# Performance work log

Hardware: AMD Instinct MI355X
Metric: run time of the kernel (lower is better)

## Reference

```python
import jax, jax.numpy as jnp
import numpy as np
import math

N_POLY = 300
N_DEG = 3
OUT_DIM = 2 * (N_DEG + 1)  # 8 sampled points per query
HEADS = 8


def _grid_sample(x, grid):
    # x: [B,C,H,W], grid: [B,Q,N,2] in [-1,1]; bilinear, zeros padding, align_corners=False
    B, C, H, W = x.shape
    ix = (grid[..., 0] + 1.0) * (W * 0.5) - 0.5
    iy = (grid[..., 1] + 1.0) * (H * 0.5) - 0.5
    ix0 = jnp.floor(ix)
    iy0 = jnp.floor(iy)
    wx1 = ix - ix0
    wy1 = iy - iy0
    x0 = ix0.astype(jnp.int32)
    y0 = iy0.astype(jnp.int32)
    xf = x.reshape(B, C, H * W)

    def gather(yc, xc):
        valid = (xc >= 0) & (xc < W) & (yc >= 0) & (yc < H)
        idx = jnp.clip(yc, 0, H - 1) * W + jnp.clip(xc, 0, W - 1)  # [B,Q,N]
        vals = jax.vmap(lambda m, i: m[:, i])(xf, idx)  # [B,C,Q,N]
        return vals * valid[:, None].astype(x.dtype)

    out = (gather(y0, x0) * ((1 - wy1) * (1 - wx1))[:, None]
           + gather(y0, x0 + 1) * ((1 - wy1) * wx1)[:, None]
           + gather(y0 + 1, x0) * (wy1 * (1 - wx1))[:, None]
           + gather(y0 + 1, x0 + 1) * (wy1 * wx1)[:, None])
    return out  # [B,C,Q,N]


def setup_inputs() -> dict:
    key = jax.random.key(0)
    B, C, H, W = 16, 256, 64, 96
    ks = list(jax.random.split(key, 20))

    def w(k, shape):
        return jax.random.normal(k, shape, jnp.float32) * (1.0 / np.sqrt(shape[0]))

    d = {}
    d['x'] = jax.random.normal(ks[0], (B, C, H, W), jnp.float32)
    d['qs_w1'] = w(ks[1], (C, 2 * C)); d['qs_b1'] = jnp.zeros((2 * C,), jnp.float32)
    d['qs_w2'] = w(ks[2], (2 * C, 1)); d['qs_b2'] = jnp.zeros((1,), jnp.float32)
    d['rp_w1'] = w(ks[3], (C, 2 * C)); d['rp_b1'] = jnp.zeros((2 * C,), jnp.float32)
    d['rp_w2'] = w(ks[4], (2 * C, OUT_DIM * 2)); d['rp_b2'] = jnp.zeros((OUT_DIM * 2,), jnp.float32)
    d['mha_in_w'] = w(ks[5], (C, 3 * C)); d['mha_in_b'] = jnp.zeros((3 * C,), jnp.float32)
    d['mha_out_w'] = w(ks[6], (C, C)); d['mha_out_b'] = jnp.zeros((C,), jnp.float32)
    d['dq_w'] = w(ks[7], (C, C)); d['dq_b'] = jnp.zeros((C,), jnp.float32)
    d['dk_w'] = w(ks[8], (C, C)); d['dk_b'] = jnp.zeros((C,), jnp.float32)
    d['dv_w'] = w(ks[9], (C, C)); d['dv_b'] = jnp.zeros((C,), jnp.float32)
    d['ln1_g'] = jnp.ones((C,), jnp.float32); d['ln1_b'] = jnp.zeros((C,), jnp.float32)
    d['cl_w1'] = w(ks[10], (C, 2 * C)); d['cl_b1'] = jnp.zeros((2 * C,), jnp.float32)
    d['cl_w2'] = w(ks[11], (2 * C, 1)); d['cl_b2'] = jnp.zeros((1,), jnp.float32)
    d['po_w1'] = w(ks[12], (C, 2 * C)); d['po_b1'] = jnp.zeros((2 * C,), jnp.float32)
    d['po_w2'] = w(ks[13], (2 * C, OUT_DIM)); d['po_b2'] = jnp.zeros((OUT_DIM,), jnp.float32)
    return d


def reference(x, qs_w1, qs_b1, qs_w2, qs_b2, rp_w1, rp_b1, rp_w2, rp_b2,
              mha_in_w, mha_in_b, mha_out_w, mha_out_b,
              dq_w, dq_b, dk_w, dk_b, dv_w, dv_b,
              ln1_g, ln1_b, cl_w1, cl_b1, cl_w2, cl_b2,
              po_w1, po_b1, po_w2, po_b2):
    B, C, H, W = x.shape
    dh = C // HEADS
    scale = 1.0 / math.sqrt(dh)

    memory = x.reshape(B, C, H * W).transpose(0, 2, 1)  # [B,HW,C]
    logits = jax.nn.elu(memory @ qs_w1 + qs_b1) @ qs_w2 + qs_b2  # [B,HW,1]
    _, idxs = jax.lax.top_k(logits[..., 0], N_POLY)  # [B,Q]
    querys = jnp.take_along_axis(memory, idxs[..., None], axis=1)  # [B,Q,C]
    rp = jnp.tanh((memory @ rp_w1 + rp_b1) @ rp_w2 + rp_b2)  # [B,HW,2*OUT_DIM]
    ref = jnp.take_along_axis(rp, idxs[..., None], axis=1).reshape(B, N_POLY, OUT_DIM, 2)

    # self-attention (nn.MultiheadAttention, batch_first, 8 heads)
    qkv = querys @ mha_in_w + mha_in_b
    q, k, v = jnp.split(qkv, 3, axis=-1)
    sh = lambda t: t.reshape(B, N_POLY, HEADS, dh).transpose(0, 2, 1, 3)
    q, k, v = sh(q), sh(k), sh(v)
    att = jax.nn.softmax(jnp.einsum('bhqd,bhkd->bhqk', q, k) * scale, axis=-1)
    o = jnp.einsum('bhqk,bhkd->bhqd', att, v).transpose(0, 2, 1, 3).reshape(B, N_POLY, C)
    o = o @ mha_out_w + mha_out_b
    tgt = querys + o  # dropout is identity in eval
    mu = tgt.mean(-1, keepdims=True)
    var = tgt.var(-1, keepdims=True)
    tgt = (tgt - mu) / jnp.sqrt(var + 1e-5) * ln1_g + ln1_b

    # deformable attention
    dq = (tgt @ dq_w + dq_b).reshape(B, N_POLY, 1, HEADS, dh).transpose(0, 1, 3, 2, 4)  # [B,Q,H,1,dh]
    samp = _grid_sample(x, ref)  # [B,C,Q,N]
    sp = samp.transpose(0, 3, 2, 1)  # [B,N,Q,C] (matches torch transpose(1,-1))
    # faithful to torch .view(B,Q,N,H,dh) on the [B,N,Q,C] contiguous tensor: plain reshape
    dk = (sp @ dk_w + dk_b).reshape(B, N_POLY, OUT_DIM, HEADS, dh).transpose(0, 1, 3, 2, 4)  # [B,Q,H,N,dh]
    dv = (sp @ dv_w + dv_b).reshape(B, N_POLY, OUT_DIM, HEADS, dh).transpose(0, 1, 3, 2, 4)
    a = jax.nn.softmax(jnp.einsum('bqhod,bqhnd->bqhon', dq, dk) * scale, axis=-1)
    out2 = jnp.einsum('bqhon,bqhnd->bqhod', a, dv).reshape(B, N_POLY, C)
    tgt = tgt + out2

    poly = jax.nn.silu(tgt @ po_w1 + po_b1) @ po_w2 + po_b2
    cls = jax.nn.sigmoid(jax.nn.elu(tgt @ cl_w1 + cl_b1) @ cl_w2 + cl_b2)[..., 0]
    return poly.reshape(B, N_POLY, 2, N_DEG + 1), cls
```

## Files before the change

kernel.cpp:

```cpp
#include <hip/hip_runtime.h>
#include <hip/hip_bf16.h>
#include <math.h>

typedef __hip_bfloat16 bf16;

#define B_   16
#define C_   256
#define H_   64
#define W_   96
#define HW_  6144
#define Q_   300
#define NH_  8
#define DH_  32
#define HID_ 512
#define QB_  4
#define SCALE_ 0.17677669529663687f

__device__ __forceinline__ float b2f(bf16 v){ return __bfloat162float(v); }
__device__ __forceinline__ bf16 f2b(float v){ return __float2bfloat16(v); }
__device__ __forceinline__ int clampi(int v, int lo, int hi){
  return v < lo ? lo : (v > hi ? hi : v);
}

__global__ __launch_bounds__(256) void xt_k(const float* __restrict__ x,
                                            float* __restrict__ xt){
  int b  = blockIdx.z;
  int c0 = blockIdx.y*64;
  int p0 = blockIdx.x*64;
  __shared__ float t[64][65];
  int tid = threadIdx.x;
  int tr = tid >> 6;
  int tc = tid & 63;
  #pragma unroll
  for (int i=0;i<16;i++){
    int cc = tr + i*4;
    t[cc][tc] = x[((size_t)b*C_ + c0+cc)*HW_ + p0 + tc];
  }
  __syncthreads();
  #pragma unroll
  for (int i=0;i<16;i++){
    int pp = tr + i*4;
    xt[((size_t)b*HW_ + p0+pp)*C_ + c0 + tc] = t[tc][pp];
  }
}

__global__ __launch_bounds__(256) void score_k(const float* __restrict__ x,
    const float* __restrict__ w1, const float* __restrict__ b1,
    const float* __restrict__ w2, const float* __restrict__ b2,
    float* __restrict__ logits){
  int b = blockIdx.y, hw0 = blockIdx.x*64;
  int tid = threadIdx.x;
  int tc = tid & 31;
  int tr = tid >> 5;
  __shared__ float xs[32][64];
  __shared__ float wsl[32][256];
  __shared__ float red[64][33];
  float part[8];
  #pragma unroll
  for (int i=0;i<8;i++) part[i]=0.f;
  for (int pass=0; pass<2; ++pass){
    float acc[8][8];
    #pragma unroll
    for (int i=0;i<8;i++)
      #pragma unroll
      for (int j=0;j<8;j++) acc[i][j]=0.f;
    for (int kt=0; kt<8; ++kt){
      #pragma unroll
      for (int i=0;i<2;i++){
        int e = tid + i*256;
        int rr4 = e & 15, kk = e >> 4;
        *reinterpret_cast<float4*>(&xs[kk][rr4*4]) =
          *reinterpret_cast<const float4*>(&x[(size_t)(b*C_ + kt*32+kk)*HW_ + hw0 + rr4*4]);
      }
      #pragma unroll
      for (int i=0;i<8;i++){
        int e = tid + i*256;
        int jj4 = e & 63, kk = e >> 6;
        *reinterpret_cast<float4*>(&wsl[kk][jj4*4]) =
          *reinterpret_cast<const float4*>(&w1[(size_t)(kt*32+kk)*HID_ + pass*256 + jj4*4]);
      }
      __syncthreads();
      #pragma unroll
      for (int k=0;k<32;k++){
        float4 a0 = *reinterpret_cast<float4*>(&xs[k][tr*8]);
        float4 a1 = *reinterpret_cast<float4*>(&xs[k][tr*8+4]);
        float4 w0 = *reinterpret_cast<float4*>(&wsl[k][tc*8]);
        float4 w4 = *reinterpret_cast<float4*>(&wsl[k][tc*8+4]);
        float aa[8] = {a0.x,a0.y,a0.z,a0.w,a1.x,a1.y,a1.z,a1.w};
        float ww[8] = {w0.x,w0.y,w0.z,w0.w,w4.x,w4.y,w4.z,w4.w};
        #pragma unroll
        for (int i=0;i<8;i++)
          #pragma unroll
          for (int j=0;j<8;j++)
            acc[i][j] += aa[i]*ww[j];
      }
      __syncthreads();
    }
    #pragma unroll
    for (int j=0;j<8;j++){
      int jg = pass*256 + tc*8 + j;
      float bb = b1[jg], w2v = w2[jg];
      #pragma unroll
      for (int i=0;i<8;i++){
        float h = acc[i][j] + bb;
        h = h > 0.f ? h : expm1f(h);
        part[i] += h * w2v;
      }
    }
  }
  #pragma unroll
  for (int i=0;i<8;i++) red[tr*8+i][tc] = part[i];
  __syncthreads();
  if (tid < 64){
    float s = 0.f;
    for (int t=0;t<32;t++) s += red[tid][t];
    logits[(size_t)b*HW_ + hw0 + tid] = s + b2[0];
  }
}

__global__ __launch_bounds__(1024) void topk_k(const float* __restrict__ logits,
                                               int* __restrict__ idxs){
  int b = blockIdx.x, tid = threadIdx.x;
  __shared__ unsigned long long keys[8192];
  for (int i = tid; i < 8192; i += 1024){
    unsigned long long key = 0ull;
    if (i < HW_){
      float v = logits[(size_t)b*HW_ + i];
      unsigned u = __float_as_uint(v);
      unsigned m = (u & 0x80000000u) ? ~u : (u ^ 0x80000000u);
      if (!(v == v)) m = 0u;
      key = ((unsigned long long)m << 32) | (unsigned)(HW_ - 1 - i);
    }
    keys[i] = key;
  }
  __syncthreads();
  for (int k = 2; k <= 8192; k <<= 1){
    for (int j = k >> 1; j >= 1; j >>= 1){
      for (int i = tid; i < 8192; i += 1024){
        int l = i ^ j;
        if (l > i){
          unsigned long long a = keys[i], c = keys[l];
          bool sw = ((i & k) == 0) ? (a < c) : (a > c);
          if (sw){ keys[i] = c; keys[l] = a; }
        }
      }
      __syncthreads();
    }
  }
  if (tid < Q_){
    int idx = HW_ - 1 - (int)(keys[tid] & 0xFFFFFFFFull);
    idxs[b*Q_ + tid] = idx;
  }
}

template<int XT>
__global__ __launch_bounds__(256) void qproj_k(const float* __restrict__ x,
    const float* __restrict__ xt,
    const int* __restrict__ idxs,
    const float* __restrict__ rw1, const float* __restrict__ rb1,
    const float* __restrict__ rw2, const float* __restrict__ rb2,
    const float* __restrict__ mw,  const float* __restrict__ mb,
    float* __restrict__ refs,
    bf16* __restrict__ qarr, bf16* __restrict__ karr, bf16* __restrict__ varr){
  int blk = blockIdx.x;
  int b = blk/(Q_/QB_), q0 = (blk%(Q_/QB_))*QB_;
  int tid = threadIdx.x;
  __shared__ float rowl[QB_][C_];
  __shared__ float hl[QB_][HID_];
  __shared__ float red[16][17];
  int idxv[QB_];
  #pragma unroll
  for (int j=0;j<QB_;j++) idxv[j] = clampi(idxs[b*Q_+q0+j], 0, HW_-1);
  #pragma unroll
  for (int j=0;j<QB_;j++){
    if (XT) rowl[j][tid] = xt[((size_t)b*HW_ + idxv[j])*C_ + tid];
    else    rowl[j][tid] = x[((size_t)b*C_ + tid)*HW_ + idxv[j]];
  }
  __syncthreads();
  float h0[QB_], h1[QB_];
  #pragma unroll
  for (int j=0;j<QB_;j++){ h0[j]=rb1[tid]; h1[j]=rb1[tid+256]; }
  for (int c=0;c<C_;c++){
    float wv0 = rw1[(size_t)c*HID_ + tid];
    float wv1 = rw1[(size_t)c*HID_ + tid + 256];
    #pragma unroll
    for (int j=0;j<QB_;j++){
      float rv = rowl[j][c];
      h0[j] += rv*wv0; h1[j] += rv*wv1;
    }
  }
  #pragma unroll
  for (int j=0;j<QB_;j++){ hl[j][tid]=h0[j]; hl[j][tid+256]=h1[j]; }
  float aq[QB_], ak[QB_], av[QB_];
  #pragma unroll
  for (int j=0;j<QB_;j++){ aq[j]=mb[tid]; ak[j]=mb[tid+256]; av[j]=mb[tid+512]; }
  for (int c=0;c<C_;c++){
    const float* wr = mw + (size_t)c*768;
    float w0 = wr[tid], w1v = wr[tid+256], w2v = wr[tid+512];
    #pragma unroll
    for (int j=0;j<QB_;j++){
      float rv = rowl[j][c];
      aq[j] += rv*w0; ak[j] += rv*w1v; av[j] += rv*w2v;
    }
  }
  int h = tid>>5, d = tid&31;
  #pragma unroll
  for (int j=0;j<QB_;j++){
    size_t o = (((size_t)b*NH_+h)*Q_+(q0+j))*DH_ + d;
    qarr[o]=f2b(aq[j]); karr[o]=f2b(ak[j]); varr[o]=f2b(av[j]);
  }
  __syncthreads();
  int o = tid & 15, seg = tid >> 4;
  for (int j=0;j<QB_;j++){
    float p = 0.f;
    for (int jj=seg*32; jj<seg*32+32; jj++) p += hl[j][jj]*rw2[jj*16+o];
    red[seg][o] = p;
    __syncthreads();
    if (tid < 16){
      float s = 0.f;
      for (int sg=0; sg<16; sg++) s += red[sg][tid];
      refs[((size_t)b*Q_+(q0+j))*16 + tid] = tanhf(s + rb2[tid]);
    }
    __syncthreads();
  }
}

__global__ __launch_bounds__(256) void attn_k(const bf16* __restrict__ qarr,
    const bf16* __restrict__ karr, const bf16* __restrict__ varr,
    bf16* __restrict__ att_o){
  int blk = blockIdx.x; int bh = blk >> 1, half = blk & 1;
  int tid = threadIdx.x, rg = tid >> 5, lane = tid & 31;
  __shared__ bf16 kk[Q_][34];
  __shared__ bf16 vv[Q_][34];
  __shared__ float ps[8][304];
  __shared__ float qsl[8][32];
  const bf16* kb = karr + (size_t)bh*Q_*DH_;
  const bf16* vb = varr + (size_t)bh*Q_*DH_;
  const bf16* qb = qarr + (size_t)bh*Q_*DH_;
  for (int e=tid; e<Q_*DH_; e+=256){
    int k = e >> 5, d = e & 31;
    kk[k][d] = kb[e];
    vv[k][d] = vb[e];
  }
  __syncthreads();
  int b = bh >> 3, h = bh & 7;
  int rbase = half*150;
  for (int p0=0; p0<150; p0+=8){
    int rr = p0 + rg;
    bool act = rr < 150;
    int r = rbase + (act ? rr : 0);
    float qd = act ? b2f(qb[r*DH_ + lane]) : 0.f;
    qsl[rg][lane] = qd;
    __syncthreads();
    float lmax = -1e30f;
    for (int k=lane; k<Q_; k+=32){
      float s = 0.f;
      #pragma unroll
      for (int d=0; d<DH_; d++) s += qsl[rg][d]*b2f(kk[k][d]);
      s *= SCALE_;
      ps[rg][k] = s;
      lmax = fmaxf(lmax, s);
    }
    #pragma unroll
    for (int off=16; off>=1; off>>=1) lmax = fmaxf(lmax, __shfl_xor(lmax, off, 32));
    float lsum = 0.f;
    for (int k=lane; k<Q_; k+=32){
      float e = expf(ps[rg][k] - lmax);
      ps[rg][k] = e;
      lsum += e;
    }
    #pragma unroll
    for (int off=16; off>=1; off>>=1) lsum += __shfl_xor(lsum, off, 32);
    __syncthreads();
    float out = 0.f;
    for (int k=0;k<Q_;k++) out += ps[rg][k]*b2f(vv[k][lane]);
    if (act) att_o[((size_t)b*Q_ + r)*C_ + h*DH_ + lane] = f2b(out / lsum);
    __syncthreads();
  }
}

template<int XT>
__global__ __launch_bounds__(256) void proj_ln_k(const bf16* __restrict__ att_o,
    const float* __restrict__ x, const float* __restrict__ xt,
    const int* __restrict__ idxs,
    const float* __restrict__ ow, const float* __restrict__ ob,
    const float* __restrict__ g,  const float* __restrict__ beta,
    const float* __restrict__ dqw, const float* __restrict__ dqb,
    float* __restrict__ tgt, float* __restrict__ dqv){
  int blk = blockIdx.x, tid = threadIdx.x;
  int b = blk/Q_, qq = blk%Q_;
  __shared__ float ol[C_];
  __shared__ float yl[C_];
  __shared__ float rs[4], rs2[4];
  size_t base = (size_t)blk*C_;
  ol[tid] = b2f(att_o[base+tid]);
  __syncthreads();
  float acc = ob[tid];
  for (int c=0;c<C_;c++) acc += ol[c]*ow[(size_t)c*C_+tid];
  int idx = clampi(idxs[b*Q_+qq], 0, HW_-1);
  float resid;
  if (XT) resid = xt[((size_t)b*HW_ + idx)*C_ + tid];
  else    resid = x[((size_t)b*C_ + tid)*HW_ + idx];
  float t = resid + acc;
  float s = t, s2 = t*t;
  #pragma unroll
  for (int off=32; off>=1; off>>=1){
    s  += __shfl_xor(s,  off, 64);
    s2 += __shfl_xor(s2, off, 64);
  }
  if ((tid&63)==0){ rs[tid>>6]=s; rs2[tid>>6]=s2; }
  __syncthreads();
  float ts=0.f, ts2=0.f;
  #pragma unroll
  for (int w=0;w<4;w++){ ts+=rs[w]; ts2+=rs2[w]; }
  float mu = ts*(1.f/256.f);
  float var = ts2*(1.f/256.f) - mu*mu;
  if (!(var > 0.f)) var = 0.f;
  float y = (t-mu)*rsqrtf(var+1e-5f)*g[tid] + beta[tid];
  tgt[base+tid] = y;
  yl[tid] = y;
  __syncthreads();
  float a2 = dqb[tid];
  for (int c=0;c<C_;c++) a2 += yl[c]*dqw[(size_t)c*C_+tid];
  dqv[base+tid] = a2;
}

template<int XT>
__global__ __launch_bounds__(256) void deform_k(const float* __restrict__ x,
    const float* __restrict__ xt,
    const float* __restrict__ refs, const float* __restrict__ dqv,
    const float* __restrict__ tgt,
    const float* __restrict__ dkw, const float* __restrict__ dkb,
    const float* __restrict__ dvw, const float* __restrict__ dvb,
    const float* __restrict__ pw1, const float* __restrict__ pb1,
    const float* __restrict__ pw2, const float* __restrict__ pb2,
    const float* __restrict__ cw1, const float* __restrict__ cb1,
    const float* __restrict__ cw2, const float* __restrict__ cb2,
    float* __restrict__ out_poly, float* __restrict__ out_cls){
  int blk = blockIdx.x; int b = blk/Q_, q2 = blk%Q_;
  int tid = threadIdx.x;
  __shared__ float rows_l[8][C_];
  __shared__ float k8[8][C_];
  __shared__ float v8[8][C_];
  __shared__ float dql[C_];
  __shared__ float tl[C_];
  __shared__ float hp[HID_];
  __shared__ float hc[HID_];
  __shared__ float redp[16][8];
  __shared__ float redc[16];
  dql[tid] = dqv[((size_t)b*Q_+q2)*C_ + tid];
  const float* xc  = x  + ((size_t)b*C_ + tid)*HW_;
  const float* xbt = xt + (size_t)b*HW_*C_;
  #pragma unroll
  for (int rr=0; rr<8; ++rr){
    int r = q2*8 + rr;
    int n = r/Q_, q = r - n*Q_;
    float gx = refs[(((size_t)b*Q_+q)*8+n)*2 + 0];
    float gy = refs[(((size_t)b*Q_+q)*8+n)*2 + 1];
    if (!(gx > -2.f && gx < 2.f)) gx = 0.f;
    if (!(gy > -2.f && gy < 2.f)) gy = 0.f;
    float ix = (gx + 1.f)*48.f - 0.5f;
    float iy = (gy + 1.f)*32.f - 0.5f;
    float fx = floorf(ix), fy = floorf(iy);
    int x0 = (int)fx, y0 = (int)fy;
    float wx1 = ix - fx, wy1 = iy - fy;
    float wx0 = 1.f - wx1, wy0 = 1.f - wy1;
    float v = 0.f;
    if (XT){
      if (y0   >= 0 && y0   < H_ && x0   >= 0 && x0   < W_) v += wy0*wx0*xbt[(size_t)(y0*W_+x0)*C_ + tid];
      if (y0   >= 0 && y0   < H_ && x0+1 >= 0 && x0+1 < W_) v += wy0*wx1*xbt[(size_t)(y0*W_+x0+1)*C_ + tid];
      if (y0+1 >= 0 && y0+1 < H_ && x0   >= 0 && x0   < W_) v += wy1*wx0*xbt[(size_t)((y0+1)*W_+x0)*C_ + tid];
      if (y0+1 >= 0 && y0+1 < H_ && x0+1 >= 0 && x0+1 < W_) v += wy1*wx1*xbt[(size_t)((y0+1)*W_+x0+1)*C_ + tid];
    } else {
      if (y0   >= 0 && y0   < H_ && x0   >= 0 && x0   < W_) v += wy0*wx0*xc[y0*W_+x0];
      if (y0   >= 0 && y0   < H_ && x0+1 >= 0 && x0+1 < W_) v += wy0*wx1*xc[y0*W_+x0+1];
      if (y0+1 >= 0 && y0+1 < H_ && x0   >= 0 && x0   < W_) v += wy1*wx0*xc[(y0+1)*W_+x0];
      if (y0+1 >= 0 && y0+1 < H_ && x0+1 >= 0 && x0+1 < W_) v += wy1*wx1*xc[(y0+1)*W_+x0+1];
    }
    rows_l[rr][tid] = v;
  }
  __syncthreads();
  float ka[8], va[8];
  float kbb = dkb[tid], vbb = dvb[tid];
  #pragma unroll
  for (int rr=0; rr<8; ++rr){ ka[rr]=kbb; va[rr]=vbb; }
  for (int c=0;c<C_;c++){
    float wk = dkw[(size_t)c*C_+tid];
    float wvv = dvw[(size_t)c*C_+tid];
    #pragma unroll
    for (int rr=0; rr<8; ++rr){
      float rv = rows_l[rr][c];
      ka[rr] += rv*wk; va[rr] += rv*wvv;
    }
  }
  #pragma unroll
  for (int rr=0; rr<8; ++rr){ k8[rr][tid]=ka[rr]; v8[rr][tid]=va[rr]; }
  __syncthreads();
  int h = tid>>5, d = tid&31;
  float qd = dql[h*DH_+d];
  float s[8];
  #pragma unroll
  for (int n=0;n<8;n++){
    float t_ = qd * k8[n][h*DH_+d];
    #pragma unroll
    for (int off=16; off>=1; off>>=1) t_ += __shfl_xor(t_, off, 32);
    s[n] = t_ * SCALE_;
  }
  float m = s[0];
  #pragma unroll
  for (int n=1;n<8;n++) m = fmaxf(m, s[n]);
  float e[8], sum = 0.f;
  #pragma unroll
  for (int n=0;n<8;n++){ e[n] = expf(s[n]-m); sum += e[n]; }
  float inv = 1.f/sum;
  float out = 0.f;
  #pragma unroll
  for (int n=0;n<8;n++) out += e[n]*inv*v8[n][h*DH_+d];
  float tv = tgt[((size_t)b*Q_+q2)*C_ + tid] + out;
  tl[tid] = tv;
  __syncthreads();
  float a0 = pb1[tid], a1 = pb1[tid+256];
  float c0 = cb1[tid], c1 = cb1[tid+256];
  for (int c=0;c<C_;c++){
    float rv = tl[c];
    a0 += rv*pw1[(size_t)c*HID_ + tid];
    a1 += rv*pw1[(size_t)c*HID_ + tid + 256];
    c0 += rv*cw1[(size_t)c*HID_ + tid];
    c1 += rv*cw1[(size_t)c*HID_ + tid + 256];
  }
  hp[tid]     = a0 * (1.f/(1.f+expf(-a0)));
  hp[tid+256] = a1 * (1.f/(1.f+expf(-a1)));
  hc[tid]     = c0 > 0.f ? c0 : expm1f(c0);
  hc[tid+256] = c1 > 0.f ? c1 : expm1f(c1);
  __syncthreads();
  if (tid < 128){
    int o = tid & 7, seg = tid >> 3;
    float p = 0.f;
    for (int j=seg*32; j<seg*32+32; j++) p += hp[j]*pw2[j*8+o];
    redp[seg][o] = p;
  } else if (tid < 144){
    int seg = tid - 128;
    float p = 0.f;
    for (int j=seg*32; j<seg*32+32; j++) p += hc[j]*cw2[j];
    redc[seg] = p;
  }
  __syncthreads();
  if (tid < 8){
    float sm = 0.f;
    for (int sg=0; sg<16; sg++) sm += redp[sg][tid];
    out_poly[((size_t)b*Q_+q2)*8 + tid] = sm + pb2[tid];
  }
  if (tid == 8){
    float sc = 0.f;
    for (int sg=0; sg<16; sg++) sc += redc[sg];
    sc += cb2[0];
    out_cls[b*Q_+q2] = 1.f/(1.f+expf(-sc));
  }
}

extern "C" void kernel_launch(void* const* d_in, const int* in_sizes, int n_in,
                              void* d_out, int out_size, void* d_ws, size_t ws_size,
                              hipStream_t stream){
  (void)in_sizes; (void)out_size;
  if (n_in < 29) return;
  const float* x       = (const float*)d_in[0];
  const float* qs_w1   = (const float*)d_in[1];
  const float* qs_b1   = (const float*)d_in[2];
  const float* qs_w2   = (const float*)d_in[3];
  const float* qs_b2   = (const float*)d_in[4];
  const float* rp_w1   = (const float*)d_in[5];
  const float* rp_b1   = (const float*)d_in[6];
  const float* rp_w2   = (const float*)d_in[7];
  const float* rp_b2   = (const float*)d_in[8];
  const float* mha_in_w  = (const float*)d_in[9];
  const float* mha_in_b  = (const float*)d_in[10];
  const float* mha_out_w = (const float*)d_in[11];
  const float* mha_out_b = (const float*)d_in[12];
  const float* dq_w    = (const float*)d_in[13];
  const float* dq_b    = (const float*)d_in[14];
  const float* dk_w    = (const float*)d_in[15];
  const float* dk_b    = (const float*)d_in[16];
  const float* dv_w    = (const float*)d_in[17];
  const float* dv_b    = (const float*)d_in[18];
  const float* ln1_g   = (const float*)d_in[19];
  const float* ln1_b   = (const float*)d_in[20];
  const float* cl_w1   = (const float*)d_in[21];
  const float* cl_b1   = (const float*)d_in[22];
  const float* cl_w2   = (const float*)d_in[23];
  const float* cl_b2   = (const float*)d_in[24];
  const float* po_w1   = (const float*)d_in[25];
  const float* po_b1   = (const float*)d_in[26];
  const float* po_w2   = (const float*)d_in[27];
  const float* po_b2   = (const float*)d_in[28];

  constexpr size_t QKV1     = (size_t)B_*NH_*Q_*DH_;
  constexpr size_t SZ_R1    = 9830400;
  constexpr size_t OFF_IDXS = SZ_R1;
  constexpr size_t OFF_REFS = OFF_IDXS + 19200;
  constexpr size_t OFF_ATTO = OFF_REFS + 307200;
  constexpr size_t WS_NEED  = OFF_ATTO + 2457600;
  constexpr size_t OFF_XT   = WS_NEED;
  constexpr size_t SZ_XT    = (size_t)B_*HW_*C_*sizeof(float);
  constexpr size_t WS_NEED2 = OFF_XT + SZ_XT;
  if (ws_size < WS_NEED) return;
  const bool use_xt = (ws_size >= WS_NEED2);

  char* ws = (char*)d_ws;
  float* logits = (float*)(ws + 0);
  bf16*  qarr   = (bf16*) (ws + 0);
  bf16*  karr   = qarr + QKV1;
  bf16*  varr   = karr + QKV1;
  float* tgt    = (float*)(ws + 0);
  float* dqv    = (float*)(ws + 4915200);
  int*   idxs   = (int*)  (ws + OFF_IDXS);
  float* refs   = (float*)(ws + OFF_REFS);
  bf16*  att_o  = (bf16*) (ws + OFF_ATTO);
  float* xt     = (float*)(ws + OFF_XT);

  float* out_poly = (float*)d_out;
  float* out_cls  = out_poly + B_*Q_*8;

  if (use_xt)
    xt_k<<<dim3(HW_/64, C_/64, B_), 256, 0, stream>>>(x, xt);

  score_k<<<dim3(HW_/64, B_), 256, 0, stream>>>(x, qs_w1, qs_b1, qs_w2, qs_b2, logits);
  topk_k<<<B_, 1024, 0, stream>>>(logits, idxs);

  if (use_xt){
    qproj_k<1><<<B_*(Q_/QB_), 256, 0, stream>>>(x, xt, idxs, rp_w1, rp_b1, rp_w2, rp_b2,
                                                mha_in_w, mha_in_b, refs, qarr, karr, varr);
  } else {
    qproj_k<0><<<B_*(Q_/QB_), 256, 0, stream>>>(x, xt, idxs, rp_w1, rp_b1, rp_w2, rp_b2,
                                                mha_in_w, mha_in_b, refs, qarr, karr, varr);
  }
  attn_k<<<B_*NH_*2, 256, 0, stream>>>(qarr, karr, varr, att_o);
  if (use_xt){
    proj_ln_k<1><<<B_*Q_, 256, 0, stream>>>(att_o, x, xt, idxs, mha_out_w, mha_out_b,
                                            ln1_g, ln1_b, dq_w, dq_b, tgt, dqv);
    deform_k<1><<<B_*Q_, 256, 0, stream>>>(x, xt, refs, dqv, tgt,
                                           dk_w, dk_b, dv_w, dv_b,
                                           po_w1, po_b1, po_w2, po_b2,
                                           cl_w1, cl_b1, cl_w2, cl_b2,
                                           out_poly, out_cls);
  } else {
    proj_ln_k<0><<<B_*Q_, 256, 0, stream>>>(att_o, x, xt, idxs, mha_out_w, mha_out_b,
                                            ln1_g, ln1_b, dq_w, dq_b, tgt, dqv);
    deform_k<0><<<B_*Q_, 256, 0, stream>>>(x, xt, refs, dqv, tgt,
                                           dk_w, dk_b, dv_w, dv_b,
                                           po_w1, po_b1, po_w2, po_b2,
                                           cl_w1, cl_b1, cl_w2, cl_b2,
                                           out_poly, out_cls);
  }
}
```

Before: 1.276 ms.

## Batch four queries per deform block and remove LDS bank conflicts in score_k

deform_k now handles QB_=4 queries per block. Each dk/dv and MLP weight load is reused across 32 sampled rows or 4 queries instead of 8 rows or 1 query. This is meant to cut the repeated global weight traffic that dominates these matrix-vector products. The cost is higher register and LDS use (32-entry accumulators) and four times fewer blocks. Separately, score_k pads the xs tile and splits each thread's weight columns into two 4-wide halves to avoid LDS bank conflicts, and it reuses the weight tile buffer for the reduction to save shared memory.

```diff
diff --git a/kernel.cpp b/kernel.cpp
--- a/kernel.cpp
+++ b/kernel.cpp
@@ -52,9 +52,9 @@
   int tid = threadIdx.x;
   int tc = tid & 31;
   int tr = tid >> 5;
-  __shared__ float xs[32][64];
+  __shared__ float xs[32][68];
   __shared__ float wsl[32][256];
-  __shared__ float red[64][33];
+  float (*red)[33] = (float(*)[33])wsl;
   float part[8];
   #pragma unroll
   for (int i=0;i<8;i++) part[i]=0.f;
@@ -84,8 +84,8 @@
       for (int k=0;k<32;k++){
         float4 a0 = *reinterpret_cast<float4*>(&xs[k][tr*8]);
         float4 a1 = *reinterpret_cast<float4*>(&xs[k][tr*8+4]);
-        float4 w0 = *reinterpret_cast<float4*>(&wsl[k][tc*8]);
-        float4 w4 = *reinterpret_cast<float4*>(&wsl[k][tc*8+4]);
+        float4 w0 = *reinterpret_cast<float4*>(&wsl[k][tc*4]);
+        float4 w4 = *reinterpret_cast<float4*>(&wsl[k][128 + tc*4]);
         float aa[8] = {a0.x,a0.y,a0.z,a0.w,a1.x,a1.y,a1.z,a1.w};
         float ww[8] = {w0.x,w0.y,w0.z,w0.w,w4.x,w4.y,w4.z,w4.w};
         #pragma unroll
@@ -98,7 +98,8 @@
     }
     #pragma unroll
     for (int j=0;j<8;j++){
-      int jg = pass*256 + tc*8 + j;
+      int col = (j < 4) ? (tc*4 + j) : (128 + tc*4 + (j-4));
+      int jg = pass*256 + col;
       float bb = b1[jg], w2v = w2[jg];
       #pragma unroll
       for (int i=0;i<8;i++){
@@ -337,23 +338,19 @@
     const float* __restrict__ cw1, const float* __restrict__ cb1,
     const float* __restrict__ cw2, const float* __restrict__ cb2,
     float* __restrict__ out_poly, float* __restrict__ out_cls){
-  int blk = blockIdx.x; int b = blk/Q_, q2 = blk%Q_;
+  int blk = blockIdx.x; int b = blk/(Q_/QB_), qg = blk%(Q_/QB_);
+  int q0 = qg*QB_;
   int tid = threadIdx.x;
-  __shared__ float rows_l[8][C_];
-  __shared__ float k8[8][C_];
-  __shared__ float v8[8][C_];
-  __shared__ float dql[C_];
-  __shared__ float tl[C_];
-  __shared__ float hp[HID_];
-  __shared__ float hc[HID_];
+  __shared__ float rows_l[32][C_];
+  __shared__ float tl[QB_][C_];
+  __shared__ float hp[QB_][HID_];
+  __shared__ float hc[QB_][HID_];
   __shared__ float redp[16][8];
   __shared__ float redc[16];
-  dql[tid] = dqv[((size_t)b*Q_+q2)*C_ + tid];
   const float* xc  = x  + ((size_t)b*C_ + tid)*HW_;
   const float* xbt = xt + (size_t)b*HW_*C_;
-  #pragma unroll
-  for (int rr=0; rr<8; ++rr){
-    int r = q2*8 + rr;
+  for (int rloc=0; rloc<32; ++rloc){
+    int r = qg*32 + rloc;
     int n = r/Q_, q = r - n*Q_;
     float gx = refs[(((size_t)b*Q_+q)*8+n)*2 + 0];
     float gy = refs[(((size_t)b*Q_+q)*8+n)*2 + 1];
@@ -377,84 +374,101 @@
       if (y0+1 >= 0 && y0+1 < H_ && x0   >= 0 && x0   < W_) v += wy1*wx0*xc[(y0+1)*W_+x0];
       if (y0+1 >= 0 && y0+1 < H_ && x0+1 >= 0 && x0+1 < W_) v += wy1*wx1*xc[(y0+1)*W_+x0+1];
     }
-    rows_l[rr][tid] = v;
-  }
-  __syncthreads();
-  float ka[8], va[8];
+    rows_l[rloc][tid] = v;
+  }
+  __syncthreads();
+  float ka[32], va[32];
   float kbb = dkb[tid], vbb = dvb[tid];
   #pragma unroll
-  for (int rr=0; rr<8; ++rr){ ka[rr]=kbb; va[rr]=vbb; }
+  for (int rr=0; rr<32; ++rr){ ka[rr]=kbb; va[rr]=vbb; }
+  for (int c=0; c<C_; c+=4){
+    float wk0 = dkw[(size_t)(c+0)*C_+tid], wk1 = dkw[(size_t)(c+1)*C_+tid];
+    float wk2 = dkw[(size_t)(c+2)*C_+tid], wk3 = dkw[(size_t)(c+3)*C_+tid];
+    float wv0 = dvw[(size_t)(c+0)*C_+tid], wv1 = dvw[(size_t)(c+1)*C_+tid];
+    float wv2 = dvw[(size_t)(c+2)*C_+tid], wv3 = dvw[(size_t)(c+3)*C_+tid];
+    #pragma unroll
+    for (int rr=0; rr<32; ++rr){
+      float4 rv = *reinterpret_cast<float4*>(&rows_l[rr][c]);
+      ka[rr] += rv.x*wk0 + rv.y*wk1 + rv.z*wk2 + rv.w*wk3;
+      va[rr] += rv.x*wv0 + rv.y*wv1 + rv.z*wv2 + rv.w*wv3;
+    }
+  }
+  #pragma unroll
+  for (int jj=0; jj<QB_; ++jj){
+    int q2 = q0 + jj;
+    float qd = dqv[((size_t)b*Q_+q2)*C_ + tid];
+    float s[8];
+    #pragma unroll
+    for (int n=0;n<8;n++){
+      float t_ = qd * ka[jj*8+n];
+      #pragma unroll
+      for (int off=16; off>=1; off>>=1) t_ += __shfl_xor(t_, off, 32);
+      s[n] = t_ * SCALE_;
+    }
+    float m = s[0];
+    #pragma unroll
+    for (int n=1;n<8;n++) m = fmaxf(m, s[n]);
+    float e[8], sum = 0.f;
+    #pragma unroll
+    for (int n=0;n<8;n++){ e[n] = expf(s[n]-m); sum += e[n]; }
+    float inv = 1.f/sum;
+    float out = 0.f;
+    #pragma unroll
+    for (int n=0;n<8;n++) out += e[n]*inv*va[jj*8+n];
+    tl[jj][tid] = tgt[((size_t)b*Q_+q2)*C_ + tid] + out;
+  }
+  __syncthreads();
+  float a0[QB_], a1[QB_], c0[QB_], c1[QB_];
+  #pragma unroll
+  for (int jj=0;jj<QB_;jj++){
+    a0[jj]=pb1[tid]; a1[jj]=pb1[tid+256];
+    c0[jj]=cb1[tid]; c1[jj]=cb1[tid+256];
+  }
   for (int c=0;c<C_;c++){
-    float wk = dkw[(size_t)c*C_+tid];
-    float wvv = dvw[(size_t)c*C_+tid];
-    #pragma unroll
-    for (int rr=0; rr<8; ++rr){
-      float rv = rows_l[rr][c];
-      ka[rr] += rv*wk; va[rr] += rv*wvv;
-    }
-  }
-  #pragma unroll
-  for (int rr=0; rr<8; ++rr){ k8[rr][tid]=ka[rr]; v8[rr][tid]=va[rr]; }
-  __syncthreads();
-  int h = tid>>5, d = tid&31;
-  float qd = dql[h*DH_+d];
-  float s[8];
-  #pragma unroll
-  for (int n=0;n<8;n++){
-    float t_ = qd * k8[n][h*DH_+d];
-    #pragma unroll
-    for (int off=16; off>=1; off>>=1) t_ += __shfl_xor(t_, off, 32);
-    s[n] = t_ * SCALE_;
-  }
-  float m = s[0];
-  #pragma unroll
-  for (int n=1;n<8;n++) m = fmaxf(m, s[n]);
-  float e[8], sum = 0.f;
-  #pragma unroll
-  for (int n=0;n<8;n++){ e[n] = expf(s[n]-m); sum += e[n]; }
-  float inv = 1.f/sum;
-  float out = 0.f;
-  #pragma unroll
-  for (int n=0;n<8;n++) out += e[n]*inv*v8[n][h*DH_+d];
-  float tv = tgt[((size_t)b*Q_+q2)*C_ + tid] + out;
-  tl[tid] = tv;
-  __syncthreads();
-  float a0 = pb1[tid], a1 = pb1[tid+256];
-  float c0 = cb1[tid], c1 = cb1[tid+256];
-  for (int c=0;c<C_;c++){
-    float rv = tl[c];
-    a0 += rv*pw1[(size_t)c*HID_ + tid];
-    a1 += rv*pw1[(size_t)c*HID_ + tid + 256];
-    c0 += rv*cw1[(size_t)c*HID_ + tid];
-    c1 += rv*cw1[(size_t)c*HID_ + tid + 256];
-  }
-  hp[tid]     = a0 * (1.f/(1.f+expf(-a0)));
-  hp[tid+256] = a1 * (1.f/(1.f+expf(-a1)));
-  hc[tid]     = c0 > 0.f ? c0 : expm1f(c0);
-  hc[tid+256] = c1 > 0.f ? c1 : expm1f(c1);
-  __syncthreads();
-  if (tid < 128){
-    int o = tid & 7, seg = tid >> 3;
-    float p = 0.f;
-    for (int j=seg*32; j<seg*32+32; j++) p += hp[j]*pw2[j*8+o];
-    redp[seg][o] = p;
-  } else if (tid < 144){
-    int seg = tid - 128;
-    float p = 0.f;
-    for (int j=seg*32; j<seg*32+32; j++) p += hc[j]*cw2[j];
-    redc[seg] = p;
-  }
-  __syncthreads();
-  if (tid < 8){
-    float sm = 0.f;
-    for (int sg=0; sg<16; sg++) sm += redp[sg][tid];
-    out_poly[((size_t)b*Q_+q2)*8 + tid] = sm + pb2[tid];
-  }
-  if (tid == 8){
-    float sc = 0.f;
-    for (int sg=0; sg<16; sg++) sc += redc[sg];
-    sc += cb2[0];
-    out_cls[b*Q_+q2] = 1.f/(1.f+expf(-sc));
+    float pwA = pw1[(size_t)c*HID_ + tid];
+    float pwB = pw1[(size_t)c*HID_ + tid + 256];
+    float cwA = cw1[(size_t)c*HID_ + tid];
+    float cwB = cw1[(size_t)c*HID_ + tid + 256];
+    #pragma unroll
+    for (int jj=0;jj<QB_;jj++){
+      float rv = tl[jj][c];
+      a0[jj] += rv*pwA; a1[jj] += rv*pwB;
+      c0[jj] += rv*cwA; c1[jj] += rv*cwB;
+    }
+  }
+  #pragma unroll
+  for (int jj=0;jj<QB_;jj++){
+    hp[jj][tid]     = a0[jj] * (1.f/(1.f+expf(-a0[jj])));
+    hp[jj][tid+256] = a1[jj] * (1.f/(1.f+expf(-a1[jj])));
+    hc[jj][tid]     = c0[jj] > 0.f ? c0[jj] : expm1f(c0[jj]);
+    hc[jj][tid+256] = c1[jj] > 0.f ? c1[jj] : expm1f(c1[jj]);
+  }
+  __syncthreads();
+  for (int jj=0;jj<QB_;jj++){
+    if (tid < 128){
+      int o = tid & 7, seg = tid >> 3;
+      float p = 0.f;
+      for (int j=seg*32; j<seg*32+32; j++) p += hp[jj][j]*pw2[j*8+o];
+      redp[seg][o] = p;
+    } else if (tid < 144){
+      int seg = tid - 128;
+      float p = 0.f;
+      for (int j=seg*32; j<seg*32+32; j++) p += hc[jj][j]*cw2[j];
+      redc[seg] = p;
+    }
+    __syncthreads();
+    if (tid < 8){
+      float sm = 0.f;
+      for (int sg=0; sg<16; sg++) sm += redp[sg][tid];
+      out_poly[((size_t)b*Q_+(q0+jj))*8 + tid] = sm + pb2[tid];
+    }
+    if (tid == 8){
+      float sc = 0.f;
+      for (int sg=0; sg<16; sg++) sc += redc[sg];
+      sc += cb2[0];
+      out_cls[b*Q_+(q0+jj)] = 1.f/(1.f+expf(-sc));
+    }
+    __syncthreads();
   }
 }
 
@@ -537,7 +551,7 @@
   if (use_xt){
     proj_ln_k<1><<<B_*Q_, 256, 0, stream>>>(att_o, x, xt, idxs, mha_out_w, mha_out_b,
                                             ln1_g, ln1_b, dq_w, dq_b, tgt, dqv);
-    deform_k<1><<<B_*Q_, 256, 0, stream>>>(x, xt, refs, dqv, tgt,
+    deform_k<1><<<B_*(Q_/QB_), 256, 0, stream>>>(x, xt, refs, dqv, tgt,
                                            dk_w, dk_b, dv_w, dv_b,
                                            po_w1, po_b1, po_w2, po_b2,
                                            cl_w1, cl_b1, cl_w2, cl_b2,
@@ -545,7 +559,7 @@
   } else {
     proj_ln_k<0><<<B_*Q_, 256, 0, stream>>>(att_o, x, xt, idxs, mha_out_w, mha_out_b,
                                             ln1_g, ln1_b, dq_w, dq_b, tgt, dqv);
-    deform_k<0><<<B_*Q_, 256, 0, stream>>>(x, xt, refs, dqv, tgt,
+    deform_k<0><<<B_*(Q_/QB_), 256, 0, stream>>>(x, xt, refs, dqv, tgt,
                                            dk_w, dk_b, dv_w, dv_b,
                                            po_w1, po_b1, po_w2, po_b2,
                                            cl_w1, cl_b1, cl_w2, cl_b2,
```

Result: slower. 1.340 ms (+5.0%).
